# Performance work log

Hardware: AMD Instinct MI355X
Metric: run time of the kernel (lower is better)

## Reference

```python
import jax, jax.numpy as jnp
import numpy as np

AU2KCALMOLA = 627.5095 * 0.529177
MAX_NRF = 100.0
N_ATOMS = 512
N_PAIRS = N_ATOMS * (N_ATOMS - 1) // 2  # 130816
BATCH = 128


def setup_inputs() -> dict:
    key = jax.random.key(0)
    k1, k2 = jax.random.split(key)
    coords = jax.random.normal(k1, (BATCH, N_ATOMS, 3), dtype=jnp.float32)
    atom_nc = jax.random.uniform(k2, (BATCH, N_PAIRS), dtype=jnp.float32)
    return {"coords": coords, "atom_nc": atom_nc}


def reference(coords, atom_nc):
    # Strict lower-triangle pair indices (row-major order == torch's
    # tril + nonzero row-major extraction order).
    n = coords.shape[1]
    ii, jj = jnp.tril_indices(n, k=-1)
    # Only compute the needed triangular pairs: [B, n_pairs, 3]
    diff = coords[:, ii, :] - coords[:, jj, :]
    d2 = jnp.sum(diff * diff, axis=-1)          # [B, n_pairs]
    r = jnp.sqrt(d2)                            # match original sqrt->square
    recip_r2 = 1.0 / (r * r)
    nrf = atom_nc * AU2KCALMOLA * recip_r2 / MAX_NRF
    return nrf
```

## Files before the change

kernel.cpp:

```cpp
#include <hip/hip_runtime.h>

#define N_ATOMS 512
#define N_PAIRS 130816
#define BATCH 128

typedef float f32x4 __attribute__((ext_vector_type(4)));

constexpr float SCALE = (float)(627.5095 * 0.529177 / 100.0);

__global__ __launch_bounds__(256) void coords_to_nrf_kernel(
    const float* __restrict__ coords,
    const float* __restrict__ atom_nc,
    float* __restrict__ out)
{
    __shared__ float c[N_ATOMS * 3];

    const int b   = blockIdx.y;
    const int blk = blockIdx.x;
    const int t   = threadIdx.x;

    {
        const f32x4* src = reinterpret_cast<const f32x4*>(coords + (size_t)b * (N_ATOMS * 3));
        f32x4* dst = reinterpret_cast<f32x4*>(c);
        for (int u = t; u < (N_ATOMS * 3) / 4; u += 256) dst[u] = src[u];
    }
    __syncthreads();

    const float* ab = atom_nc + (size_t)b * N_PAIRS;
    float*       ob = out     + (size_t)b * N_PAIRS;

    float a[8], xj[8], yj[8], zj[8], xi[8], yi[8], zi[8];
    int   pp[8];

    #pragma unroll
    for (int m = 0; m < 4; ++m) {
        const int k  = blk * 4 + m;
        const int i1 = k;
        const int i2 = 511 - k;
        const int base1 = (i1 * (i1 - 1)) / 2;
        const int base2 = (i2 * (i2 - 1)) / 2;
        const float xi1 = c[3 * i1], yi1 = c[3 * i1 + 1], zi1 = c[3 * i1 + 2];
        const float xi2 = c[3 * i2], yi2 = c[3 * i2 + 1], zi2 = c[3 * i2 + 2];

        #pragma unroll
        for (int u = 0; u < 2; ++u) {
            const int r = m * 2 + u;
            const int idx = min(u * 256 + t, 510);
            const bool first = idx < i1;
            const int  j = first ? idx : idx - i1;
            pp[r] = (first ? base1 : base2) + j;
            xi[r] = first ? xi1 : xi2;
            yi[r] = first ? yi1 : yi2;
            zi[r] = first ? zi1 : zi2;
            xj[r] = c[3 * j];
            yj[r] = c[3 * j + 1];
            zj[r] = c[3 * j + 2];
            a[r]  = ab[pp[r]];
        }
    }

    #pragma unroll
    for (int r = 0; r < 8; ++r) {
        const float dx = xi[r] - xj[r];
        const float dy = yi[r] - yj[r];
        const float dz = zi[r] - zj[r];
        const float d2 = dx * dx + dy * dy + dz * dz;
        const float res = a[r] * SCALE * __builtin_amdgcn_rcpf(d2);
        __builtin_nontemporal_store(res, &ob[pp[r]]);
    }
}

extern "C" void kernel_launch(void* const* d_in, const int* in_sizes, int n_in,
                              void* d_out, int out_size, void* d_ws, size_t ws_size,
                              hipStream_t stream) {
    const float* coords  = (const float*)d_in[0];
    const float* atom_nc = (const float*)d_in[1];
    float* out = (float*)d_out;

    dim3 block(256);
    dim3 grid(64, BATCH);
    coords_to_nrf_kernel<<<grid, block, 0, stream>>>(coords, atom_nc, out);
}
```

Before: 27.96 us.

## Issue atom_nc loads before coords staging and split shared coords into xy/z arrays

New measurement: 28.25 us. No clear change (+1.0%).

```diff
diff --git a/kernel.cpp b/kernel.cpp
--- a/kernel.cpp
+++ b/kernel.cpp
@@ -4,7 +4,7 @@
 #define N_PAIRS 130816
 #define BATCH 128
 
-typedef float f32x4 __attribute__((ext_vector_type(4)));
+typedef float f32x2 __attribute__((ext_vector_type(2)));
 
 constexpr float SCALE = (float)(627.5095 * 0.529177 / 100.0);
 
@@ -13,25 +13,18 @@
     const float* __restrict__ atom_nc,
     float* __restrict__ out)
 {
-    __shared__ float c[N_ATOMS * 3];
+    __shared__ f32x2 cxy[N_ATOMS];
+    __shared__ float cz [N_ATOMS];
 
     const int b   = blockIdx.y;
     const int blk = blockIdx.x;
     const int t   = threadIdx.x;
 
-    {
-        const f32x4* src = reinterpret_cast<const f32x4*>(coords + (size_t)b * (N_ATOMS * 3));
-        f32x4* dst = reinterpret_cast<f32x4*>(c);
-        for (int u = t; u < (N_ATOMS * 3) / 4; u += 256) dst[u] = src[u];
-    }
-    __syncthreads();
-
     const float* ab = atom_nc + (size_t)b * N_PAIRS;
     float*       ob = out     + (size_t)b * N_PAIRS;
 
-    float a[8], xj[8], yj[8], zj[8], xi[8], yi[8], zi[8];
-    int   pp[8];
-
+    int pp[8], jj[8];
+    bool ff[8];
     #pragma unroll
     for (int m = 0; m < 4; ++m) {
         const int k  = blk * 4 + m;
@@ -39,31 +32,52 @@
         const int i2 = 511 - k;
         const int base1 = (i1 * (i1 - 1)) / 2;
         const int base2 = (i2 * (i2 - 1)) / 2;
-        const float xi1 = c[3 * i1], yi1 = c[3 * i1 + 1], zi1 = c[3 * i1 + 2];
-        const float xi2 = c[3 * i2], yi2 = c[3 * i2 + 1], zi2 = c[3 * i2 + 2];
-
         #pragma unroll
         for (int u = 0; u < 2; ++u) {
             const int r = m * 2 + u;
-            const int idx = min(u * 256 + t, 510);
+            const int idx = (u == 0) ? t : min(256 + t, 510);
             const bool first = idx < i1;
-            const int  j = first ? idx : idx - i1;
-            pp[r] = (first ? base1 : base2) + j;
-            xi[r] = first ? xi1 : xi2;
-            yi[r] = first ? yi1 : yi2;
-            zi[r] = first ? zi1 : zi2;
-            xj[r] = c[3 * j];
-            yj[r] = c[3 * j + 1];
-            zj[r] = c[3 * j + 2];
-            a[r]  = ab[pp[r]];
+            ff[r] = first;
+            jj[r] = first ? idx : idx - i1;
+            pp[r] = (first ? base1 : base2) + jj[r];
         }
+    }
+
+    float a[8];
+    #pragma unroll
+    for (int r = 0; r < 8; ++r) a[r] = ab[pp[r]];
+
+    {
+        const float* cb = coords + (size_t)b * (N_ATOMS * 3);
+        #pragma unroll
+        for (int s = 0; s < 2; ++s) {
+            const int atom = s * 256 + t;
+            f32x2 v; v.x = cb[3 * atom]; v.y = cb[3 * atom + 1];
+            cxy[atom] = v;
+            cz [atom] = cb[3 * atom + 2];
+        }
+    }
+    __syncthreads();
+
+    f32x2 ixy1[4], ixy2[4];
+    float iz1[4], iz2[4];
+    #pragma unroll
+    for (int m = 0; m < 4; ++m) {
+        const int k = blk * 4 + m;
+        ixy1[m] = cxy[k];       iz1[m] = cz[k];
+        ixy2[m] = cxy[511 - k]; iz2[m] = cz[511 - k];
     }
 
     #pragma unroll
     for (int r = 0; r < 8; ++r) {
-        const float dx = xi[r] - xj[r];
-        const float dy = yi[r] - yj[r];
-        const float dz = zi[r] - zj[r];
+        const int m = r >> 1;
+        const f32x2 jxy = cxy[jj[r]];
+        const float jz  = cz [jj[r]];
+        const f32x2 ixy = ff[r] ? ixy1[m] : ixy2[m];
+        const float iz  = ff[r] ? iz1[m]  : iz2[m];
+        const float dx = ixy.x - jxy.x;
+        const float dy = ixy.y - jxy.y;
+        const float dz = iz    - jz;
         const float d2 = dx * dx + dy * dy + dz * dz;
         const float res = a[r] * SCALE * __builtin_amdgcn_rcpf(d2);
         __builtin_nontemporal_store(res, &ob[pp[r]]);
```
